# Kernel optimization log

Measured on AMD Instinct MI355X. Metric: run time of the kernel, lower is better.

Reference implementation:

```python
import jax, jax.numpy as jnp
import numpy as np

SIGMA = 0.1
B_PARAM = 1.0
EPS_NORM = 1e-12  # torch F.normalize eps
EPS_MIN = 1e-5


def setup_inputs() -> dict:
    key = jax.random.key(0)
    k1, k2 = jax.random.split(key)
    x = jax.random.normal(k1, (4, 64, 64, 64), dtype=jnp.float32)
    y = jax.random.normal(k2, (4, 64, 64, 64), dtype=jnp.float32)
    return {"x": x, "y": y}


def reference(x, y):
    B, C, H, W = x.shape
    N = H * W
    xf = x.reshape(B, C, N)
    yf = y.reshape(B, C, N)
    # F.normalize along channel dim (L2, eps-clamped denominator)
    xn = xf / jnp.maximum(jnp.linalg.norm(xf, axis=1, keepdims=True), EPS_NORM)
    yn = yf / jnp.maximum(jnp.linalg.norm(yf, axis=1, keepdims=True), EPS_NORM)
    xt = jnp.transpose(xn, (0, 2, 1))  # [B, N, C]
    yt = jnp.transpose(yn, (0, 2, 1))  # [B, N, C]
    x2 = jnp.sum(xt * xt, axis=-1, keepdims=True)          # [B, N, 1]
    y2 = jnp.sum(yt * yt, axis=-1)[:, None, :]             # [B, 1, N]
    d2 = x2 + y2 - 2.0 * jnp.einsum('bnc,bmc->bnm', xt, yt)  # [B, N, N]
    dist = jnp.sqrt(jnp.maximum(d2, 0.0))
    d_min = jnp.min(dist, axis=-1, keepdims=True)
    d_scaled = dist / (d_min + EPS_MIN)
    w = jnp.exp((B_PARAM - d_scaled) / SIGMA)
    cx = w / jnp.sum(w, axis=-1, keepdims=True)
    cx_max = jnp.max(cx, axis=-1)  # [B, N]
    return -jnp.log(jnp.mean(cx_max + EPS_MIN))
```

## Files before the change

kernel.cpp:

```cpp
#include <hip/hip_runtime.h>
#include <math.h>

constexpr int B_   = 4;
constexpr int C_   = 64;
constexpr int HW   = 4096;
constexpr int ROWS = B_ * HW;

constexpr float SIGMA    = 0.1f;
constexpr float EPS_MIN  = 1e-5f;
constexpr float EPS_NORM = 1e-12f;
constexpr float LOG2E    = 1.44269504088896340736f;

constexpr int CC = 512;
constexpr int SR = 64;
constexpr int NS = CC / SR;
constexpr int XR = 256;

using short8  = __attribute__((ext_vector_type(8))) short;
using floatx4 = __attribute__((ext_vector_type(4))) float;

__device__ inline ushort f2bf(float f) {
    unsigned u = __float_as_uint(f);
    unsigned r = u + 0x7FFFu + ((u >> 16) & 1u);
    return (ushort)(r >> 16);
}

__global__ __launch_bounds__(256) void nrm_kernel(const float* __restrict__ x,
                                                  const float* __restrict__ y,
                                                  ushort* __restrict__ xn,
                                                  ushort* __restrict__ yn,
                                                  unsigned* __restrict__ dmin_u,
                                                  float* __restrict__ S) {
    int p = blockIdx.x * 256 + threadIdx.x;
    if (p < ROWS) { dmin_u[p] = 0x7F800000u; S[p] = 0.0f; }
    const float* src; ushort* dst; int q;
    if (p < ROWS) { src = x; dst = xn; q = p; }
    else          { src = y; dst = yn; q = p - ROWS; }
    int b = q >> 12;
    int n = q & (HW - 1);
    const float* base = src + ((size_t)b * C_) * HW + n;
    float v[C_];
    float ss = 0.0f;
#pragma unroll
    for (int c = 0; c < C_; ++c) {
        v[c] = base[(size_t)c * HW];
        ss = fmaf(v[c], v[c], ss);
    }
    float scale = 1.0f / fmaxf(sqrtf(ss), EPS_NORM);
    short8* o = (short8*)(dst + (size_t)q * C_);
#pragma unroll
    for (int c8 = 0; c8 < C_ / 8; ++c8) {
        short8 pk;
#pragma unroll
        for (int j = 0; j < 8; ++j) pk[j] = (short)f2bf(v[c8 * 8 + j] * scale);
        o[c8] = pk;
    }
}

template <int PASS>
__global__ __launch_bounds__(256, 2) void gemm_pass(const ushort* __restrict__ xn,
                                                    const ushort* __restrict__ yn,
                                                    unsigned* __restrict__ dmin_u,
                                                    float* __restrict__ S) {
    __shared__ short8 lds[2][SR * 8];

    int tid  = threadIdx.x;
    int wid  = tid >> 6;
    int lane = tid & 63;
    int lrow = lane & 15;
    int kgrp = lane >> 4;

    int b     = blockIdx.z;
    int nbase = blockIdx.y * XR + wid * 64;
    int cbase = blockIdx.x * CC;

    const ushort* xb = xn + (size_t)(b * HW + nbase) * C_;
    const short8* yv = (const short8*)(yn + (size_t)(b * HW + cbase) * C_);

    short8 xb0[4], xb1[4];
#pragma unroll
    for (int xt = 0; xt < 4; ++xt) {
        xb0[xt] = *(const short8*)(xb + (xt * 16 + lrow) * C_ + kgrp * 8);
        xb1[xt] = *(const short8*)(xb + (xt * 16 + lrow) * C_ + 32 + kgrp * 8);
    }

    int row0 = b * HW + nbase + lrow;

    int wrow = tid >> 3, wslot = tid & 7;
    int w0 = wrow * 8 + (wslot ^ (wrow & 7));
    int w1 = (wrow + 32) * 8 + (wslot ^ (wrow & 7));

    float st[4];
    float kk2[4], c02[4];
    if (PASS == 0) {
#pragma unroll
        for (int xt = 0; xt < 4; ++xt) st[xt] = -INFINITY;
    } else {
#pragma unroll
        for (int xt = 0; xt < 4; ++xt) {
            float dm = __uint_as_float(dmin_u[row0 + xt * 16]);
            kk2[xt] = LOG2E / (SIGMA * (dm + EPS_MIN));
            c02[xt] = dm * kk2[xt];
            st[xt]  = 0.0f;
        }
    }

    {
        short8 v0 = yv[tid], v1 = yv[tid + 256];
        lds[0][w0] = v0;
        lds[0][w1] = v1;
    }
    __syncthreads();

    for (int s = 0; s < NS; ++s) {
        int cur = s & 1;
        short8 n0, n1;
        if (s + 1 < NS) {
            n0 = yv[(s + 1) * 512 + tid];
            n1 = yv[(s + 1) * 512 + 256 + tid];
        }
#pragma unroll
        for (int yt = 0; yt < 4; ++yt) {
            int p = yt * 16 + lrow;
            int q = p & 7;
            short8 ya0 = lds[cur][p * 8 + (kgrp ^ q)];
            short8 ya1 = lds[cur][p * 8 + ((kgrp + 4) ^ q)];
#pragma unroll
            for (int xt = 0; xt < 4; ++xt) {
                floatx4 acc = {0.0f, 0.0f, 0.0f, 0.0f};
                acc = __builtin_amdgcn_mfma_f32_16x16x32_bf16(ya0, xb0[xt], acc, 0, 0, 0);
                acc = __builtin_amdgcn_mfma_f32_16x16x32_bf16(ya1, xb1[xt], acc, 0, 0, 0);
                if (PASS == 0) {
                    st[xt] = fmaxf(st[xt],
                             fmaxf(fmaxf(acc[0], acc[1]), fmaxf(acc[2], acc[3])));
                } else {
#pragma unroll
                    for (int r = 0; r < 4; ++r) {
                        float d2 = fmaxf(fmaf(-2.0f, acc[r], 2.0f), 0.0f);
                        float d  = __builtin_amdgcn_sqrtf(d2);
                        st[xt] += __builtin_amdgcn_exp2f(fmaf(-kk2[xt], d, c02[xt]));
                    }
                }
            }
        }
        if (s + 1 < NS) {
            lds[cur ^ 1][w0] = n0;
            lds[cur ^ 1][w1] = n1;
        }
        __syncthreads();
    }

#pragma unroll
    for (int off = 16; off < 64; off <<= 1) {
#pragma unroll
        for (int xt = 0; xt < 4; ++xt) {
            float o = __shfl_xor(st[xt], off);
            st[xt] = (PASS == 0) ? fmaxf(st[xt], o) : (st[xt] + o);
        }
    }
    if (kgrp == 0) {
#pragma unroll
        for (int xt = 0; xt < 4; ++xt) {
            int row = row0 + xt * 16;
            if (PASS == 0) {
                float d2 = fmaxf(fmaf(-2.0f, st[xt], 2.0f), 0.0f);
                float d  = sqrtf(d2);
                atomicMin(&dmin_u[row], __float_as_uint(d));
            } else {
                atomicAdd(&S[row], st[xt]);
            }
        }
    }
}

__global__ __launch_bounds__(256) void final_kernel(const float* __restrict__ S,
                                                    float* __restrict__ out) {
    const float4* S4 = (const float4*)S;
    float acc = 0.0f;
    for (int i = threadIdx.x; i < ROWS / 4; i += 256) {
        float4 v = S4[i];
        acc += __builtin_amdgcn_rcpf(v.x) + __builtin_amdgcn_rcpf(v.y) +
               __builtin_amdgcn_rcpf(v.z) + __builtin_amdgcn_rcpf(v.w) +
               4.0f * EPS_MIN;
    }
#pragma unroll
    for (int off = 32; off > 0; off >>= 1)
        acc += __shfl_down(acc, off);
    __shared__ float part[4];
    if ((threadIdx.x & 63) == 0) part[threadIdx.x >> 6] = acc;
    __syncthreads();
    if (threadIdx.x == 0) {
        float t = part[0] + part[1] + part[2] + part[3];
        out[0] = -logf(t / (float)ROWS);
    }
}

extern "C" void kernel_launch(void* const* d_in, const int* in_sizes, int n_in,
                              void* d_out, int out_size, void* d_ws, size_t ws_size,
                              hipStream_t stream) {
    const float* x = (const float*)d_in[0];
    const float* y = (const float*)d_in[1];
    float* out = (float*)d_out;

    char* ws = (char*)d_ws;
    size_t nrm_bytes = (size_t)ROWS * C_ * sizeof(ushort);
    ushort*   xn     = (ushort*)(ws);
    ushort*   yn     = (ushort*)(ws + nrm_bytes);
    unsigned* dmin_u = (unsigned*)(ws + 2 * nrm_bytes);
    float*    S      = (float*)(ws + 2 * nrm_bytes + (size_t)ROWS * sizeof(unsigned));

    hipLaunchKernelGGL(nrm_kernel, dim3(2 * ROWS / 256), dim3(256), 0, stream,
                       x, y, xn, yn, dmin_u, S);
    dim3 grid(HW / CC, HW / XR, B_);
    hipLaunchKernelGGL(gemm_pass<0>, grid, dim3(256), 0, stream,
                       xn, yn, dmin_u, S);
    hipLaunchKernelGGL(gemm_pass<1>, grid, dim3(256), 0, stream,
                       xn, yn, dmin_u, S);
    hipLaunchKernelGGL(final_kernel, dim3(1), dim3(256), 0, stream, S, out);
}
```

Before: 100.5 us.

## Fuse min and softmax-sum passes into one kernel with per-wave y slices

Merges the two GEMM passes into one kernel. Each block owns 32 x rows and its four waves each sweep a quarter of the y columns through private LDS double buffers, so no block-wide barriers are needed inside the loop. The row minimum is combined in LDS and reused by the second sweep in the same block, and per-row reciprocals are summed into one global scalar. This removes the dmin/S global arrays, the per-row atomics and the separate reduction pass. In exchange the x-tile reuse per y load is smaller (32 rows instead of 256), so y traffic from L2 goes up, and every block now does both sweeps back to back.

```diff
diff --git a/kernel.cpp b/kernel.cpp
--- a/kernel.cpp
+++ b/kernel.cpp
@@ -11,10 +11,10 @@
 constexpr float EPS_NORM = 1e-12f;
 constexpr float LOG2E    = 1.44269504088896340736f;
 
-constexpr int CC = 512;
-constexpr int SR = 64;
-constexpr int NS = CC / SR;
-constexpr int XR = 256;
+constexpr int XR  = 32;
+constexpr int YQ  = HW / 4;
+constexpr int SRW = 64;
+constexpr int NSW = YQ / SRW;
 
 using short8  = __attribute__((ext_vector_type(8))) short;
 using floatx4 = __attribute__((ext_vector_type(4))) float;
@@ -29,10 +29,9 @@
                                                   const float* __restrict__ y,
                                                   ushort* __restrict__ xn,
                                                   ushort* __restrict__ yn,
-                                                  unsigned* __restrict__ dmin_u,
-                                                  float* __restrict__ S) {
+                                                  float* __restrict__ total) {
     int p = blockIdx.x * 256 + threadIdx.x;
-    if (p < ROWS) { dmin_u[p] = 0x7F800000u; S[p] = 0.0f; }
+    if (p == 0) *total = 0.0f;
     const float* src; ushort* dst; int q;
     if (p < ROWS) { src = x; dst = xn; q = p; }
     else          { src = y; dst = yn; q = p - ROWS; }
@@ -57,142 +56,149 @@
     }
 }
 
-template <int PASS>
-__global__ __launch_bounds__(256, 2) void gemm_pass(const ushort* __restrict__ xn,
-                                                    const ushort* __restrict__ yn,
-                                                    unsigned* __restrict__ dmin_u,
-                                                    float* __restrict__ S) {
-    __shared__ short8 lds[2][SR * 8];
-
-    int tid  = threadIdx.x;
-    int wid  = tid >> 6;
-    int lane = tid & 63;
-    int lrow = lane & 15;
-    int kgrp = lane >> 4;
-
-    int b     = blockIdx.z;
-    int nbase = blockIdx.y * XR + wid * 64;
-    int cbase = blockIdx.x * CC;
+__global__ __launch_bounds__(256, 2) void main_kernel(const ushort* __restrict__ xn,
+                                                      const ushort* __restrict__ yn,
+                                                      float* __restrict__ total) {
+    __shared__ short8 stg[4][2][SRW * 8];
+    __shared__ float  red[4][XR];
+    __shared__ float  dmf[XR];
+
+    const int tid  = threadIdx.x;
+    const int wid  = tid >> 6;
+    const int lane = tid & 63;
+    const int lrow = lane & 15;
+    const int kgrp = lane >> 4;
+
+    const int blk   = blockIdx.x;
+    const int b     = blk >> 7;
+    const int nbase = (blk & 127) * XR;
 
     const ushort* xb = xn + (size_t)(b * HW + nbase) * C_;
-    const short8* yv = (const short8*)(yn + (size_t)(b * HW + cbase) * C_);
-
-    short8 xb0[4], xb1[4];
-#pragma unroll
-    for (int xt = 0; xt < 4; ++xt) {
-        xb0[xt] = *(const short8*)(xb + (xt * 16 + lrow) * C_ + kgrp * 8);
-        xb1[xt] = *(const short8*)(xb + (xt * 16 + lrow) * C_ + 32 + kgrp * 8);
-    }
-
-    int row0 = b * HW + nbase + lrow;
-
-    int wrow = tid >> 3, wslot = tid & 7;
-    int w0 = wrow * 8 + (wslot ^ (wrow & 7));
-    int w1 = (wrow + 32) * 8 + (wslot ^ (wrow & 7));
-
-    float st[4];
-    float kk2[4], c02[4];
-    if (PASS == 0) {
-#pragma unroll
-        for (int xt = 0; xt < 4; ++xt) st[xt] = -INFINITY;
-    } else {
-#pragma unroll
-        for (int xt = 0; xt < 4; ++xt) {
-            float dm = __uint_as_float(dmin_u[row0 + xt * 16]);
-            kk2[xt] = LOG2E / (SIGMA * (dm + EPS_MIN));
-            c02[xt] = dm * kk2[xt];
-            st[xt]  = 0.0f;
-        }
-    }
-
-    {
-        short8 v0 = yv[tid], v1 = yv[tid + 256];
-        lds[0][w0] = v0;
-        lds[0][w1] = v1;
-    }
+    short8 xf0[2], xf1[2];
+#pragma unroll
+    for (int xt = 0; xt < 2; ++xt) {
+        xf0[xt] = *(const short8*)(xb + (xt * 16 + lrow) * C_ + kgrp * 8);
+        xf1[xt] = *(const short8*)(xb + (xt * 16 + lrow) * C_ + 32 + kgrp * 8);
+    }
+
+    const short8* yq = (const short8*)(yn + (size_t)(b * HW + wid * YQ) * C_);
+    const int wbase = (lane >> 3) * 8 + ((lane & 7) ^ (lane >> 3));
+
+    short8 v[8];
+    float st0[2] = {-INFINITY, -INFINITY};
+
+#pragma unroll
+    for (int g = 0; g < 8; ++g) v[g] = yq[g * 64 + lane];
+#pragma unroll
+    for (int g = 0; g < 8; ++g) stg[wid][0][g * 64 + wbase] = v[g];
+
+    for (int s = 0; s < NSW; ++s) {
+        int cur = s & 1;
+        if (s + 1 < NSW) {
+#pragma unroll
+            for (int g = 0; g < 8; ++g) v[g] = yq[(s + 1) * 512 + g * 64 + lane];
+        }
+#pragma unroll
+        for (int yt = 0; yt < 4; ++yt) {
+            int p = yt * 16 + lrow, q = p & 7;
+            short8 ya0 = stg[wid][cur][p * 8 + (kgrp ^ q)];
+            short8 ya1 = stg[wid][cur][p * 8 + ((kgrp + 4) ^ q)];
+#pragma unroll
+            for (int xt = 0; xt < 2; ++xt) {
+                floatx4 acc = {0.0f, 0.0f, 0.0f, 0.0f};
+                acc = __builtin_amdgcn_mfma_f32_16x16x32_bf16(ya0, xf0[xt], acc, 0, 0, 0);
+                acc = __builtin_amdgcn_mfma_f32_16x16x32_bf16(ya1, xf1[xt], acc, 0, 0, 0);
+                st0[xt] = fmaxf(st0[xt],
+                          fmaxf(fmaxf(acc[0], acc[1]), fmaxf(acc[2], acc[3])));
+            }
+        }
+        if (s + 1 < NSW) {
+#pragma unroll
+            for (int g = 0; g < 8; ++g) stg[wid][cur ^ 1][g * 64 + wbase] = v[g];
+        }
+    }
+
+#pragma unroll
+    for (int off = 16; off < 64; off <<= 1) {
+        st0[0] = fmaxf(st0[0], __shfl_xor(st0[0], off));
+        st0[1] = fmaxf(st0[1], __shfl_xor(st0[1], off));
+    }
+    if (kgrp == 0) { red[wid][lrow] = st0[0]; red[wid][16 + lrow] = st0[1]; }
     __syncthreads();
-
-    for (int s = 0; s < NS; ++s) {
+    if (tid < XR) {
+        float m = fmaxf(fmaxf(red[0][tid], red[1][tid]),
+                        fmaxf(red[2][tid], red[3][tid]));
+        dmf[tid] = sqrtf(fmaxf(fmaf(-2.0f, m, 2.0f), 0.0f));
+    }
+    __syncthreads();
+
+    float kk2[2], c02[2];
+#pragma unroll
+    for (int xt = 0; xt < 2; ++xt) {
+        float dm = dmf[xt * 16 + lrow];
+        kk2[xt] = LOG2E / (SIGMA * (dm + EPS_MIN));
+        c02[xt] = dm * kk2[xt];
+    }
+
+    float s2[2] = {0.0f, 0.0f};
+#pragma unroll
+    for (int g = 0; g < 8; ++g) v[g] = yq[g * 64 + lane];
+#pragma unroll
+    for (int g = 0; g < 8; ++g) stg[wid][0][g * 64 + wbase] = v[g];
+
+    for (int s = 0; s < NSW; ++s) {
         int cur = s & 1;
-        short8 n0, n1;
-        if (s + 1 < NS) {
-            n0 = yv[(s + 1) * 512 + tid];
-            n1 = yv[(s + 1) * 512 + 256 + tid];
+        if (s + 1 < NSW) {
+#pragma unroll
+            for (int g = 0; g < 8; ++g) v[g] = yq[(s + 1) * 512 + g * 64 + lane];
         }
 #pragma unroll
         for (int yt = 0; yt < 4; ++yt) {
-            int p = yt * 16 + lrow;
-            int q = p & 7;
-            short8 ya0 = lds[cur][p * 8 + (kgrp ^ q)];
-            short8 ya1 = lds[cur][p * 8 + ((kgrp + 4) ^ q)];
-#pragma unroll
-            for (int xt = 0; xt < 4; ++xt) {
+            int p = yt * 16 + lrow, q = p & 7;
+            short8 ya0 = stg[wid][cur][p * 8 + (kgrp ^ q)];
+            short8 ya1 = stg[wid][cur][p * 8 + ((kgrp + 4) ^ q)];
+#pragma unroll
+            for (int xt = 0; xt < 2; ++xt) {
                 floatx4 acc = {0.0f, 0.0f, 0.0f, 0.0f};
-                acc = __builtin_amdgcn_mfma_f32_16x16x32_bf16(ya0, xb0[xt], acc, 0, 0, 0);
-                acc = __builtin_amdgcn_mfma_f32_16x16x32_bf16(ya1, xb1[xt], acc, 0, 0, 0);
-                if (PASS == 0) {
-                    st[xt] = fmaxf(st[xt],
-                             fmaxf(fmaxf(acc[0], acc[1]), fmaxf(acc[2], acc[3])));
-                } else {
-#pragma unroll
-                    for (int r = 0; r < 4; ++r) {
-                        float d2 = fmaxf(fmaf(-2.0f, acc[r], 2.0f), 0.0f);
-                        float d  = __builtin_amdgcn_sqrtf(d2);
-                        st[xt] += __builtin_amdgcn_exp2f(fmaf(-kk2[xt], d, c02[xt]));
-                    }
+                acc = __builtin_amdgcn_mfma_f32_16x16x32_bf16(ya0, xf0[xt], acc, 0, 0, 0);
+                acc = __builtin_amdgcn_mfma_f32_16x16x32_bf16(ya1, xf1[xt], acc, 0, 0, 0);
+#pragma unroll
+                for (int r = 0; r < 4; ++r) {
+                    float d2 = fmaxf(fmaf(-2.0f, acc[r], 2.0f), 0.0f);
+                    float d  = __builtin_amdgcn_sqrtf(d2);
+                    s2[xt] += __builtin_amdgcn_exp2f(fmaf(-kk2[xt], d, c02[xt]));
                 }
             }
         }
-        if (s + 1 < NS) {
-            lds[cur ^ 1][w0] = n0;
-            lds[cur ^ 1][w1] = n1;
-        }
-        __syncthreads();
+        if (s + 1 < NSW) {
+#pragma unroll
+            for (int g = 0; g < 8; ++g) stg[wid][cur ^ 1][g * 64 + wbase] = v[g];
+        }
     }
 
 #pragma unroll
     for (int off = 16; off < 64; off <<= 1) {
-#pragma unroll
-        for (int xt = 0; xt < 4; ++xt) {
-            float o = __shfl_xor(st[xt], off);
-            st[xt] = (PASS == 0) ? fmaxf(st[xt], o) : (st[xt] + o);
-        }
-    }
-    if (kgrp == 0) {
-#pragma unroll
-        for (int xt = 0; xt < 4; ++xt) {
-            int row = row0 + xt * 16;
-            if (PASS == 0) {
-                float d2 = fmaxf(fmaf(-2.0f, st[xt], 2.0f), 0.0f);
-                float d  = sqrtf(d2);
-                atomicMin(&dmin_u[row], __float_as_uint(d));
-            } else {
-                atomicAdd(&S[row], st[xt]);
-            }
-        }
-    }
-}
-
-__global__ __launch_bounds__(256) void final_kernel(const float* __restrict__ S,
-                                                    float* __restrict__ out) {
-    const float4* S4 = (const float4*)S;
-    float acc = 0.0f;
-    for (int i = threadIdx.x; i < ROWS / 4; i += 256) {
-        float4 v = S4[i];
-        acc += __builtin_amdgcn_rcpf(v.x) + __builtin_amdgcn_rcpf(v.y) +
-               __builtin_amdgcn_rcpf(v.z) + __builtin_amdgcn_rcpf(v.w) +
-               4.0f * EPS_MIN;
-    }
-#pragma unroll
-    for (int off = 32; off > 0; off >>= 1)
-        acc += __shfl_down(acc, off);
-    __shared__ float part[4];
-    if ((threadIdx.x & 63) == 0) part[threadIdx.x >> 6] = acc;
+        s2[0] += __shfl_xor(s2[0], off);
+        s2[1] += __shfl_xor(s2[1], off);
+    }
+    if (kgrp == 0) { red[wid][lrow] = s2[0]; red[wid][16 + lrow] = s2[1]; }
     __syncthreads();
-    if (threadIdx.x == 0) {
-        float t = part[0] + part[1] + part[2] + part[3];
-        out[0] = -logf(t / (float)ROWS);
-    }
+
+    if (tid < 64) {
+        float acc = 0.0f;
+        if (tid < XR) {
+            float Ssum = red[0][tid] + red[1][tid] + red[2][tid] + red[3][tid];
+            acc = __builtin_amdgcn_rcpf(Ssum) + EPS_MIN;
+        }
+#pragma unroll
+        for (int off = 16; off > 0; off >>= 1) acc += __shfl_down(acc, off);
+        if (tid == 0) atomicAdd(total, acc);
+    }
+}
+
+__global__ void final_kernel(const float* __restrict__ total,
+                             float* __restrict__ out) {
+    out[0] = -logf(total[0] / (float)ROWS);
 }
 
 extern "C" void kernel_launch(void* const* d_in, const int* in_sizes, int n_in,
@@ -204,17 +210,13 @@
 
     char* ws = (char*)d_ws;
     size_t nrm_bytes = (size_t)ROWS * C_ * sizeof(ushort);
-    ushort*   xn     = (ushort*)(ws);
-    ushort*   yn     = (ushort*)(ws + nrm_bytes);
-    unsigned* dmin_u = (unsigned*)(ws + 2 * nrm_bytes);
-    float*    S      = (float*)(ws + 2 * nrm_bytes + (size_t)ROWS * sizeof(unsigned));
+    ushort* xn    = (ushort*)(ws);
+    ushort* yn    = (ushort*)(ws + nrm_bytes);
+    float*  total = (float*)(ws + 2 * nrm_bytes);
 
     hipLaunchKernelGGL(nrm_kernel, dim3(2 * ROWS / 256), dim3(256), 0, stream,
-                       x, y, xn, yn, dmin_u, S);
-    dim3 grid(HW / CC, HW / XR, B_);
-    hipLaunchKernelGGL(gemm_pass<0>, grid, dim3(256), 0, stream,
-                       xn, yn, dmin_u, S);
-    hipLaunchKernelGGL(gemm_pass<1>, grid, dim3(256), 0, stream,
-                       xn, yn, dmin_u, S);
-    hipLaunchKernelGGL(final_kernel, dim3(1), dim3(256), 0, stream, S, out);
-}
+                       x, y, xn, yn, total);
+    hipLaunchKernelGGL(main_kernel, dim3(ROWS / XR), dim3(256), 0, stream,
+                       xn, yn, total);
+    hipLaunchKernelGGL(final_kernel, dim3(1), dim3(1), 0, stream, total, out);
+}
```

Result: no change. 101.1 us (+0.5%).
